# Performance work log

Hardware: AMD Instinct MI355X
Metric: run time of the kernel (lower is better)

## Reference

```python
import jax, jax.numpy as jnp
import numpy as np

N, E = 50000, 800000
DIN, FIN, H, DN, FE = 128, 7, 4, 64, 32
NEG_SLOPE = 0.01  # torch leaky_relu default


def setup_inputs() -> dict:
    key = jax.random.key(0)
    ks = jax.random.split(key, 8)
    nfeats = jax.random.normal(ks[0], (N, DIN), dtype=jnp.float32)
    efeats = jax.random.uniform(ks[1], (E, FIN), dtype=jnp.float32)
    src = jax.random.randint(ks[2], (E,), 0, N, dtype=jnp.int32)
    dst = jax.random.randint(ks[3], (E,), 0, N, dtype=jnp.int32)
    # parameters (xavier-normal-ish scale), stored in jax [in, out] layout
    W_nodes = jax.random.normal(ks[4], (DIN, H * DN), dtype=jnp.float32) * (2.0 / (DIN + H * DN)) ** 0.5
    b_nodes = jnp.zeros((H * DN,), dtype=jnp.float32)
    W_edges = jax.random.normal(ks[5], (FIN + 2 * DIN, H * FE), dtype=jnp.float32) * (2.0 / (FIN + 2 * DIN + H * FE)) ** 0.5
    W_attn = jax.random.normal(ks[6], (H, FE), dtype=jnp.float32) * (2.0 / (FE + H)) ** 0.5  # torch [out,in] layout
    return {"nfeats": nfeats, "efeats": efeats, "src": src, "dst": dst,
            "W_nodes": W_nodes, "b_nodes": b_nodes, "W_edges": W_edges, "W_attn": W_attn}


def reference(nfeats, efeats, src, dst, W_nodes, b_nodes, W_edges, W_attn):
    n = nfeats.shape[0]
    e = efeats.shape[0]
    h_heads = W_attn.shape[0]
    # node projection: [N, H, DN]
    h = (nfeats @ W_nodes + b_nodes).reshape(n, h_heads, -1)
    # per-edge feature MLP on [h_src || f || h_dst]  (raw node feats, as in edge_attention)
    stack = jnp.concatenate([nfeats[src], efeats, nfeats[dst]], axis=-1)  # [E, FIN+2*DIN]
    f_out = jax.nn.leaky_relu(stack @ W_edges, NEG_SLOPE).reshape(e, h_heads, -1)  # [E, H, FE]
    # a = fc_attn(f_out).sum(-1): sums over both attn output heads and FE
    a = jnp.einsum('ehj,kj->eh', f_out, W_attn)  # [E, H]
    # segment (per-destination) softmax, numerically stable
    amax = jax.ops.segment_max(a, dst, num_segments=n)          # [N, H]
    ex = jnp.exp(a - amax[dst])                                 # [E, H]
    denom = jax.ops.segment_sum(ex, dst, num_segments=n)       # [N, H]
    alpha = ex / denom[dst]                                     # [E, H]
    # weighted aggregation of projected src features
    msg = alpha[:, :, None] * h[src]                            # [E, H, DN]
    h_out = jax.ops.segment_sum(msg, dst, num_segments=n)      # [N, H, DN]
    return h_out, f_out
```

## Files before the change

kernel.cpp:

```cpp
#include <hip/hip_runtime.h>

#define NEG_SLOPE 0.01f

typedef __attribute__((ext_vector_type(8))) __bf16 bf16x8;
typedef __attribute__((ext_vector_type(4))) float  f32x4;

__device__ __forceinline__ unsigned short f2bf(float x) {
    unsigned u; __builtin_memcpy(&u, &x, 4);
    unsigned r = u + 0x7FFFu + ((u >> 16) & 1u);
    return (unsigned short)(r >> 16);
}
__device__ __forceinline__ float bflo(unsigned u) {
    unsigned v = u << 16; float f; __builtin_memcpy(&f, &v, 4); return f;
}
__device__ __forceinline__ float bfhi(unsigned u) {
    unsigned v = u & 0xFFFF0000u; float f; __builtin_memcpy(&f, &v, 4); return f;
}

__global__ void zero_kernel(int* __restrict__ p, int n) {
    int i = blockIdx.x * blockDim.x + threadIdx.x;
    if (i < n) p[i] = 0;
}

__global__ __launch_bounds__(256) void bt_prep(
    const float* __restrict__ Wn, const float* __restrict__ We,
    short* __restrict__ Btg)
{
    int idx = blockIdx.x * 256 + threadIdx.x;
    int n = idx >> 7, k = idx & 127;
    float v;
    if (n < 256)      v = Wn[(size_t)k * 256 + n];
    else if (n < 384) v = We[(size_t)k * 128 + (n - 256)];
    else              v = We[(size_t)(135 + k) * 128 + (n - 384)];
    Btg[(size_t)n * 128 + k] = (short)f2bf(v);
}

__global__ __launch_bounds__(256) void gemm_mfma(
    const float* __restrict__ A, const float* __restrict__ bn,
    const short* __restrict__ Btg, unsigned short* __restrict__ hbf,
    unsigned short* __restrict__ Pbf, unsigned short* __restrict__ Qbf, int N)
{
    __shared__ __align__(16) short Al[128 * 136];
    __shared__ __align__(16) short Bl[128 * 136];
    int t = threadIdx.x;
    int row0 = blockIdx.x * 128;

    #pragma unroll
    for (int i = 0; i < 16; i++) {
        int idx = t + i * 256;
        int fr = idx >> 5, fc4 = idx & 31;
        int row = row0 + fr;
        float4 v = make_float4(0.f, 0.f, 0.f, 0.f);
        if (row < N) v = *(const float4*)(A + (size_t)row * 128 + fc4 * 4);
        unsigned long long pk =  (unsigned long long)f2bf(v.x)
                              | ((unsigned long long)f2bf(v.y) << 16)
                              | ((unsigned long long)f2bf(v.z) << 32)
                              | ((unsigned long long)f2bf(v.w) << 48);
        *(unsigned long long*)&Al[fr * 136 + fc4 * 4] = pk;
    }
    __syncthreads();

    int w = t >> 6, l = t & 63;
    int lr = l & 15, lg = l >> 4;

    for (int ct = 0; ct < 4; ct++) {
        if (ct > 0) __syncthreads();
        #pragma unroll
        for (int i = 0; i < 8; i++) {
            int idx = t + i * 256;
            int r = idx >> 4, c8 = idx & 15;
            uint4 v = *(const uint4*)(Btg + (size_t)(ct * 128 + r) * 128 + c8 * 8);
            *(uint4*)&Bl[r * 136 + c8 * 8] = v;
        }
        __syncthreads();

        f32x4 acc[2][8];
        #pragma unroll
        for (int fr = 0; fr < 2; fr++)
            #pragma unroll
            for (int fc = 0; fc < 8; fc++) {
                acc[fr][fc][0] = 0.f; acc[fr][fc][1] = 0.f;
                acc[fr][fc][2] = 0.f; acc[fr][fc][3] = 0.f;
            }

        #pragma unroll
        for (int ks = 0; ks < 4; ks++) {
            int k0 = ks * 32 + lg * 8;
            bf16x8 a0 = *(const bf16x8*)&Al[(w * 32 + lr) * 136 + k0];
            bf16x8 a1 = *(const bf16x8*)&Al[(w * 32 + 16 + lr) * 136 + k0];
            #pragma unroll
            for (int fc = 0; fc < 8; fc++) {
                bf16x8 bb = *(const bf16x8*)&Bl[(fc * 16 + lr) * 136 + k0];
                acc[0][fc] = __builtin_amdgcn_mfma_f32_16x16x32_bf16(a0, bb, acc[0][fc], 0, 0, 0);
                acc[1][fc] = __builtin_amdgcn_mfma_f32_16x16x32_bf16(a1, bb, acc[1][fc], 0, 0, 0);
            }
        }

        #pragma unroll
        for (int fc = 0; fc < 8; fc++) {
            int col = fc * 16 + lr;
            float bias = (ct < 2) ? bn[ct * 128 + col] : 0.f;
            #pragma unroll
            for (int fr = 0; fr < 2; fr++) {
                #pragma unroll
                for (int b = 0; b < 4; b++) {
                    int row = row0 + w * 32 + fr * 16 + lg * 4 + b;
                    if (row >= N) continue;
                    unsigned short bv = f2bf(acc[fr][fc][b] + bias);
                    if (ct < 2)       hbf[(size_t)row * 256 + ct * 128 + col] = bv;
                    else if (ct == 2) Pbf[(size_t)row * 128 + col] = bv;
                    else              Qbf[(size_t)row * 128 + col] = bv;
                }
            }
        }
    }
}

__global__ void count_kernel(const int* __restrict__ dst, int* __restrict__ deg, int E) {
    int i = blockIdx.x * blockDim.x + threadIdx.x;
    if (i < E) atomicAdd(&deg[dst[i]], 1);
}

__global__ __launch_bounds__(256) void scan_sum(
    const int* __restrict__ deg, int* __restrict__ bsum, int n)
{
    int b = blockIdx.x, t = threadIdx.x;
    int base = b * 1024 + t * 4;
    int s = 0;
    #pragma unroll
    for (int k = 0; k < 4; k++) { int i = base + k; if (i < n) s += deg[i]; }
    #pragma unroll
    for (int off = 32; off >= 1; off >>= 1) s += __shfl_xor(s, off);
    __shared__ int ws[4];
    if ((t & 63) == 0) ws[t >> 6] = s;
    __syncthreads();
    if (t == 0) bsum[b] = ws[0] + ws[1] + ws[2] + ws[3];
}

__global__ void scan_offsets(const int* __restrict__ bsum, int* __restrict__ boff,
                             int nb, int* __restrict__ row_start, int n)
{
    int acc = 0;
    for (int b = 0; b < nb; b++) { boff[b] = acc; acc += bsum[b]; }
    row_start[n] = acc;
}

__global__ __launch_bounds__(256) void scan_write(
    const int* __restrict__ deg, const int* __restrict__ boff,
    int* __restrict__ row_start, int* __restrict__ cursor, int n)
{
    int b = blockIdx.x, t = threadIdx.x, lane = t & 63, w = t >> 6;
    int base = b * 1024 + t * 4;
    int x0, x1, x2, x3;
    x0 = (base + 0 < n) ? deg[base + 0] : 0;
    x1 = (base + 1 < n) ? deg[base + 1] : 0;
    x2 = (base + 2 < n) ? deg[base + 2] : 0;
    x3 = (base + 3 < n) ? deg[base + 3] : 0;
    int tsum = x0 + x1 + x2 + x3;
    int inc = tsum;
    #pragma unroll
    for (int off = 1; off < 64; off <<= 1) {
        int v = __shfl_up(inc, off);
        if (lane >= off) inc += v;
    }
    int texcl = inc - tsum;
    __shared__ int wsum[4];
    if (lane == 63) wsum[w] = inc;
    __syncthreads();
    int wexcl = 0;
    #pragma unroll
    for (int ww = 0; ww < 4; ww++) if (ww < w) wexcl += wsum[ww];
    int basev = boff[b] + wexcl + texcl;
    int p0 = basev;
    int p1 = p0 + x0;
    int p2 = p1 + x1;
    int p3 = p2 + x2;
    if (base + 0 < n) { row_start[base + 0] = p0; cursor[base + 0] = p0; }
    if (base + 1 < n) { row_start[base + 1] = p1; cursor[base + 1] = p1; }
    if (base + 2 < n) { row_start[base + 2] = p2; cursor[base + 2] = p2; }
    if (base + 3 < n) { row_start[base + 3] = p3; cursor[base + 3] = p3; }
}

__global__ void scatter_kernel(const int* __restrict__ dst, const int* __restrict__ src,
                               int* __restrict__ cursor, int2* __restrict__ es, int E) {
    int i = blockIdx.x * blockDim.x + threadIdx.x;
    if (i < E) {
        int pos = atomicAdd(&cursor[dst[i]], 1);
        es[pos] = make_int2(i, src[i]);
    }
}

__global__ __launch_bounds__(256) void fused_kernel(
    const int* __restrict__ row_start, const int2* __restrict__ ES,
    const float* __restrict__ ef,
    const unsigned short* __restrict__ Pbf, const unsigned short* __restrict__ Qbf,
    const unsigned short* __restrict__ hbf,
    const float* __restrict__ We, const float* __restrict__ Wa,
    float* __restrict__ f_out, float* __restrict__ out, int N)
{
    int t = threadIdx.x;
    int lane = t & 63;
    int n = (int)((blockIdx.x * blockDim.x + t) >> 6);
    if (n >= N) return;
    int c0 = lane * 2;

    float4* O4 = (float4*)out;
    int nu = __builtin_amdgcn_readfirstlane(n);
    int start = row_start[nu];
    int deg   = row_start[nu + 1] - start;
    if (deg == 0) {
        O4[(size_t)n * 64 + lane] = make_float4(0.f, 0.f, 0.f, 0.f);
        return;
    }

    float wf0[7], wf1[7];
    #pragma unroll
    for (int j = 0; j < 7; j++) {
        wf0[j] = We[(size_t)(128 + j) * 128 + c0];
        wf1[j] = We[(size_t)(128 + j) * 128 + c0 + 1];
    }
    int j0 = c0 & 31, j1 = j0 + 1;
    float wv0 = Wa[j0] + Wa[32 + j0] + Wa[64 + j0] + Wa[96 + j0];
    float wv1 = Wa[j1] + Wa[32 + j1] + Wa[64 + j1] + Wa[96 + j1];

    const unsigned* P1 = (const unsigned*)Pbf;
    const uint2*    H2 = (const uint2*)hbf;

    unsigned qu = ((const unsigned*)Qbf)[(size_t)n * 64 + lane];
    float q0 = bflo(qu), q1 = bfhi(qu);

    #define DSTR(X) \
        float m##X = -1e30f, d##X = 0.f;                                  \
        float4 a##X = make_float4(0.f, 0.f, 0.f, 0.f);                    \
        int e##X = 0; unsigned pu##X = 0; uint2 hu##X = make_uint2(0u,0u);\
        float f##X##0=0.f,f##X##1=0.f,f##X##2=0.f,f##X##3=0.f,            \
              f##X##4=0.f,f##X##5=0.f,f##X##6=0.f;
    #define DNXT(X) \
        int e##X = 0; unsigned pu##X = 0; uint2 hu##X = make_uint2(0u,0u);\
        float f##X##0=0.f,f##X##1=0.f,f##X##2=0.f,f##X##3=0.f,            \
              f##X##4=0.f,f##X##5=0.f,f##X##6=0.f;

    #define LOADE(pos, X) {                                               \
        int p_ = start + (pos);                                           \
        int2 es_ = ES[p_];                                                \
        e##X = __builtin_amdgcn_readfirstlane(es_.x);                     \
        int s_ = __builtin_amdgcn_readfirstlane(es_.y);                   \
        pu##X = P1[(size_t)s_ * 64 + lane];                               \
        hu##X = H2[(size_t)s_ * 64 + lane];                               \
        const float* ep_ = ef + (size_t)e##X * 7;                         \
        f##X##0 = ep_[0]; f##X##1 = ep_[1]; f##X##2 = ep_[2];             \
        f##X##3 = ep_[3]; f##X##4 = ep_[4]; f##X##5 = ep_[5];             \
        f##X##6 = ep_[6]; }

    #define PROC(X) {                                                     \
        float a0 = bflo(pu##X) + q0, a1 = bfhi(pu##X) + q1;               \
        a0 = fmaf(f##X##0, wf0[0], a0); a1 = fmaf(f##X##0, wf1[0], a1);   \
        a0 = fmaf(f##X##1, wf0[1], a0); a1 = fmaf(f##X##1, wf1[1], a1);   \
        a0 = fmaf(f##X##2, wf0[2], a0); a1 = fmaf(f##X##2, wf1[2], a1);   \
        a0 = fmaf(f##X##3, wf0[3], a0); a1 = fmaf(f##X##3, wf1[3], a1);   \
        a0 = fmaf(f##X##4, wf0[4], a0); a1 = fmaf(f##X##4, wf1[4], a1);   \
        a0 = fmaf(f##X##5, wf0[5], a0); a1 = fmaf(f##X##5, wf1[5], a1);   \
        a0 = fmaf(f##X##6, wf0[6], a0); a1 = fmaf(f##X##6, wf1[6], a1);   \
        float v0 = a0 > 0.f ? a0 : NEG_SLOPE * a0;                        \
        float v1 = a1 > 0.f ? a1 : NEG_SLOPE * a1;                        \
        float2 fv_ = make_float2(v0, v1);                                 \
        unsigned long long u_;                                            \
        __builtin_memcpy(&u_, &fv_, 8);                                   \
        __builtin_nontemporal_store(u_,                                   \
            (unsigned long long*)(f_out + (size_t)e##X * 128 + c0));      \
        float p_ = fmaf(v0, wv0, v1 * wv1);                               \
        p_ += __shfl_xor(p_, 8);                                          \
        p_ += __shfl_xor(p_, 4);                                          \
        p_ += __shfl_xor(p_, 2);                                          \
        p_ += __shfl_xor(p_, 1);                                          \
        float nm_ = fmaxf(m##X, p_);                                      \
        float sc_ = __expf(m##X - nm_);                                   \
        float pe_ = __expf(p_ - nm_);                                     \
        d##X = d##X * sc_ + pe_;                                          \
        float hx0 = bflo(hu##X.x), hx1 = bfhi(hu##X.x);                   \
        float hx2 = bflo(hu##X.y), hx3 = bfhi(hu##X.y);                   \
        a##X.x = fmaf(a##X.x, sc_, pe_ * hx0);                            \
        a##X.y = fmaf(a##X.y, sc_, pe_ * hx1);                            \
        a##X.z = fmaf(a##X.z, sc_, pe_ * hx2);                            \
        a##X.w = fmaf(a##X.w, sc_, pe_ * hx3);                            \
        m##X = nm_; }

    #define ROT(X, Y) { e##X = e##Y; pu##X = pu##Y; hu##X = hu##Y;        \
        f##X##0 = f##Y##0; f##X##1 = f##Y##1; f##X##2 = f##Y##2;          \
        f##X##3 = f##Y##3; f##X##4 = f##Y##4; f##X##5 = f##Y##5;          \
        f##X##6 = f##Y##6; }

    DSTR(A) DSTR(B) DSTR(C) DSTR(D)

    LOADE(0, A);
    if (deg > 1) LOADE(1, B);
    if (deg > 2) LOADE(2, C);
    if (deg > 3) LOADE(3, D);

    for (int k = 0;; k++) {
        int base = 4 * k;
        DNXT(An) DNXT(Bn) DNXT(Cn) DNXT(Dn)
        if (base + 4 < deg) LOADE(base + 4, An);
        if (base + 5 < deg) LOADE(base + 5, Bn);
        if (base + 6 < deg) LOADE(base + 6, Cn);
        if (base + 7 < deg) LOADE(base + 7, Dn);

        PROC(A);
        if (base + 1 < deg) PROC(B);
        if (base + 2 < deg) PROC(C);
        if (base + 3 < deg) PROC(D);

        if (base + 4 >= deg) break;
        ROT(A, An); ROT(B, Bn); ROT(C, Cn); ROT(D, Dn);
    }

    float nm = fmaxf(fmaxf(mA, mB), fmaxf(mC, mD));
    float scA = __expf(mA - nm), scB = __expf(mB - nm);
    float scC = __expf(mC - nm), scD = __expf(mD - nm);
    float den = dA * scA + dB * scB + dC * scC + dD * scD;
    float r = 1.f / den;
    float4 acc;
    acc.x = (aA.x * scA + aB.x * scB + aC.x * scC + aD.x * scD) * r;
    acc.y = (aA.y * scA + aB.y * scB + aC.y * scC + aD.y * scD) * r;
    acc.z = (aA.z * scA + aB.z * scB + aC.z * scC + aD.z * scD) * r;
    acc.w = (aA.w * scA + aB.w * scB + aC.w * scC + aD.w * scD) * r;
    O4[(size_t)n * 64 + lane] = acc;

    #undef DSTR
    #undef DNXT
    #undef LOADE
    #undef PROC
    #undef ROT
}

extern "C" void kernel_launch(void* const* d_in, const int* in_sizes, int n_in,
                              void* d_out, int out_size, void* d_ws, size_t ws_size,
                              hipStream_t stream)
{
    const float* nfeats = (const float*)d_in[0];
    const float* efeats = (const float*)d_in[1];
    const int*   src    = (const int*)d_in[2];
    const int*   dst    = (const int*)d_in[3];
    const float* Wn     = (const float*)d_in[4];
    const float* bn     = (const float*)d_in[5];
    const float* We     = (const float*)d_in[6];
    const float* Wa     = (const float*)d_in[7];

    int N = in_sizes[0] / 128;
    int E = in_sizes[2];

    char* ws = (char*)d_ws;
    size_t off = 0;
    unsigned short* hbf = (unsigned short*)(ws + off); off += (size_t)N * 256 * 2;
    unsigned short* Pbf = (unsigned short*)(ws + off); off += (size_t)N * 128 * 2;
    unsigned short* Qbf = (unsigned short*)(ws + off); off += (size_t)N * 128 * 2;
    short* Btg   = (short*)(ws + off); off += (size_t)512 * 128 * 2;
    int2* es       = (int2*)(ws + off); off += (size_t)E * 8;
    int* deg       = (int*)(ws + off); off += (size_t)(N + 1) * 4;
    int* row_start = (int*)(ws + off); off += (size_t)(N + 1) * 4;
    int* cursor    = (int*)(ws + off); off += (size_t)(N + 1) * 4;
    int* bsum      = (int*)(ws + off); off += 1024;
    int* boff      = (int*)(ws + off); off += 1024;

    float* h_out = (float*)d_out;
    float* f_out = (float*)d_out + (size_t)N * 256;

    zero_kernel<<<(N + 255) / 256, 256, 0, stream>>>(deg, N);

    bt_prep<<<256, 256, 0, stream>>>(Wn, We, Btg);
    gemm_mfma<<<(N + 127) / 128, 256, 0, stream>>>(nfeats, bn, Btg, hbf, Pbf, Qbf, N);

    count_kernel<<<(E + 255) / 256, 256, 0, stream>>>(dst, deg, E);

    int nb = (N + 1023) / 1024;
    scan_sum<<<nb, 256, 0, stream>>>(deg, bsum, N);
    scan_offsets<<<1, 1, 0, stream>>>(bsum, boff, nb, row_start, N);
    scan_write<<<nb, 256, 0, stream>>>(deg, boff, row_start, cursor, N);

    scatter_kernel<<<(E + 255) / 256, 256, 0, stream>>>(dst, src, cursor, es, E);

    fused_kernel<<<(N + 3) / 4, 256, 0, stream>>>(row_start, es, efeats,
                                                  Pbf, Qbf, hbf, We, Wa,
                                                  f_out, h_out, N);
}
```

Measured before the change: 327.3 us.

## Interleave P and h rows into one buffer and split GEMM over column tiles

The per-source projections P (128 bf16) and h (256 bf16) now sit in one interleaved row of 384 bf16. Each lane fetches its P pair and h quad with a single 12-byte load, so the gather in the edge loop touches one contiguous region per source node. The GEMM grid also becomes 2D with 64-row tiles and one column tile per block, which gives more blocks and more parallelism, but each column tile reloads and reconverts the A rows. The interleaved write pattern scatters 2-byte stores and the 12-byte gather loads may not be aligned.

```diff
diff --git a/kernel.cpp b/kernel.cpp
--- a/kernel.cpp
+++ b/kernel.cpp
@@ -37,16 +37,17 @@
 
 __global__ __launch_bounds__(256) void gemm_mfma(
     const float* __restrict__ A, const float* __restrict__ bn,
-    const short* __restrict__ Btg, unsigned short* __restrict__ hbf,
-    unsigned short* __restrict__ Pbf, unsigned short* __restrict__ Qbf, int N)
-{
-    __shared__ __align__(16) short Al[128 * 136];
+    const short* __restrict__ Btg, unsigned short* __restrict__ PH,
+    unsigned short* __restrict__ Qbf, int N)
+{
+    __shared__ __align__(16) short Al[64 * 136];
     __shared__ __align__(16) short Bl[128 * 136];
     int t = threadIdx.x;
-    int row0 = blockIdx.x * 128;
-
-    #pragma unroll
-    for (int i = 0; i < 16; i++) {
+    int ct = blockIdx.y;
+    int row0 = blockIdx.x * 64;
+
+    #pragma unroll
+    for (int i = 0; i < 8; i++) {
         int idx = t + i * 256;
         int fr = idx >> 5, fc4 = idx & 31;
         int row = row0 + fr;
@@ -58,59 +59,51 @@
                               | ((unsigned long long)f2bf(v.w) << 48);
         *(unsigned long long*)&Al[fr * 136 + fc4 * 4] = pk;
     }
+    #pragma unroll
+    for (int i = 0; i < 8; i++) {
+        int idx = t + i * 256;
+        int r = idx >> 4, c8 = idx & 15;
+        uint4 v = *(const uint4*)(Btg + (size_t)(ct * 128 + r) * 128 + c8 * 8);
+        *(uint4*)&Bl[r * 136 + c8 * 8] = v;
+    }
     __syncthreads();
 
     int w = t >> 6, l = t & 63;
     int lr = l & 15, lg = l >> 4;
 
-    for (int ct = 0; ct < 4; ct++) {
-        if (ct > 0) __syncthreads();
-        #pragma unroll
-        for (int i = 0; i < 8; i++) {
-            int idx = t + i * 256;
-            int r = idx >> 4, c8 = idx & 15;
-            uint4 v = *(const uint4*)(Btg + (size_t)(ct * 128 + r) * 128 + c8 * 8);
-            *(uint4*)&Bl[r * 136 + c8 * 8] = v;
-        }
-        __syncthreads();
-
-        f32x4 acc[2][8];
-        #pragma unroll
-        for (int fr = 0; fr < 2; fr++)
-            #pragma unroll
-            for (int fc = 0; fc < 8; fc++) {
-                acc[fr][fc][0] = 0.f; acc[fr][fc][1] = 0.f;
-                acc[fr][fc][2] = 0.f; acc[fr][fc][3] = 0.f;
-            }
-
-        #pragma unroll
-        for (int ks = 0; ks < 4; ks++) {
-            int k0 = ks * 32 + lg * 8;
-            bf16x8 a0 = *(const bf16x8*)&Al[(w * 32 + lr) * 136 + k0];
-            bf16x8 a1 = *(const bf16x8*)&Al[(w * 32 + 16 + lr) * 136 + k0];
-            #pragma unroll
-            for (int fc = 0; fc < 8; fc++) {
-                bf16x8 bb = *(const bf16x8*)&Bl[(fc * 16 + lr) * 136 + k0];
-                acc[0][fc] = __builtin_amdgcn_mfma_f32_16x16x32_bf16(a0, bb, acc[0][fc], 0, 0, 0);
-                acc[1][fc] = __builtin_amdgcn_mfma_f32_16x16x32_bf16(a1, bb, acc[1][fc], 0, 0, 0);
-            }
-        }
-
+    f32x4 acc[8];
+    #pragma unroll
+    for (int fc = 0; fc < 8; fc++) {
+        acc[fc][0] = 0.f; acc[fc][1] = 0.f; acc[fc][2] = 0.f; acc[fc][3] = 0.f;
+    }
+
+    #pragma unroll
+    for (int ks = 0; ks < 4; ks++) {
+        int k0 = ks * 32 + lg * 8;
+        bf16x8 a0 = *(const bf16x8*)&Al[(w * 16 + lr) * 136 + k0];
         #pragma unroll
         for (int fc = 0; fc < 8; fc++) {
-            int col = fc * 16 + lr;
-            float bias = (ct < 2) ? bn[ct * 128 + col] : 0.f;
-            #pragma unroll
-            for (int fr = 0; fr < 2; fr++) {
-                #pragma unroll
-                for (int b = 0; b < 4; b++) {
-                    int row = row0 + w * 32 + fr * 16 + lg * 4 + b;
-                    if (row >= N) continue;
-                    unsigned short bv = f2bf(acc[fr][fc][b] + bias);
-                    if (ct < 2)       hbf[(size_t)row * 256 + ct * 128 + col] = bv;
-                    else if (ct == 2) Pbf[(size_t)row * 128 + col] = bv;
-                    else              Qbf[(size_t)row * 128 + col] = bv;
-                }
+            bf16x8 bb = *(const bf16x8*)&Bl[(fc * 16 + lr) * 136 + k0];
+            acc[fc] = __builtin_amdgcn_mfma_f32_16x16x32_bf16(a0, bb, acc[fc], 0, 0, 0);
+        }
+    }
+
+    #pragma unroll
+    for (int fc = 0; fc < 8; fc++) {
+        int col = fc * 16 + lr;
+        float bias = (ct < 2) ? bn[ct * 128 + col] : 0.f;
+        #pragma unroll
+        for (int b = 0; b < 4; b++) {
+            int row = row0 + w * 16 + lg * 4 + b;
+            if (row >= N) continue;
+            unsigned short bv = f2bf(acc[fc][b] + bias);
+            if (ct < 2) {
+                int col256 = ct * 128 + col;
+                PH[(size_t)row * 384 + (col256 >> 2) * 6 + 2 + (col256 & 3)] = bv;
+            } else if (ct == 2) {
+                PH[(size_t)row * 384 + (col >> 1) * 6 + (col & 1)] = bv;
+            } else {
+                Qbf[(size_t)row * 128 + col] = bv;
             }
         }
     }
@@ -193,8 +186,7 @@
 __global__ __launch_bounds__(256) void fused_kernel(
     const int* __restrict__ row_start, const int2* __restrict__ ES,
     const float* __restrict__ ef,
-    const unsigned short* __restrict__ Pbf, const unsigned short* __restrict__ Qbf,
-    const unsigned short* __restrict__ hbf,
+    const unsigned short* __restrict__ PH, const unsigned short* __restrict__ Qbf,
     const float* __restrict__ We, const float* __restrict__ Wa,
     float* __restrict__ f_out, float* __restrict__ out, int N)
 {
@@ -222,9 +214,6 @@
     int j0 = c0 & 31, j1 = j0 + 1;
     float wv0 = Wa[j0] + Wa[32 + j0] + Wa[64 + j0] + Wa[96 + j0];
     float wv1 = Wa[j1] + Wa[32 + j1] + Wa[64 + j1] + Wa[96 + j1];
-
-    const unsigned* P1 = (const unsigned*)Pbf;
-    const uint2*    H2 = (const uint2*)hbf;
 
     unsigned qu = ((const unsigned*)Qbf)[(size_t)n * 64 + lane];
     float q0 = bflo(qu), q1 = bfhi(qu);
@@ -245,8 +234,9 @@
         int2 es_ = ES[p_];                                                \
         e##X = __builtin_amdgcn_readfirstlane(es_.x);                     \
         int s_ = __builtin_amdgcn_readfirstlane(es_.y);                   \
-        pu##X = P1[(size_t)s_ * 64 + lane];                               \
-        hu##X = H2[(size_t)s_ * 64 + lane];                               \
+        uint3 ph_ = *(const uint3*)(PH + (size_t)s_ * 384 + lane * 6);    \
+        pu##X = ph_.x;                                                    \
+        hu##X = make_uint2(ph_.y, ph_.z);                                 \
         const float* ep_ = ef + (size_t)e##X * 7;                         \
         f##X##0 = ep_[0]; f##X##1 = ep_[1]; f##X##2 = ep_[2];             \
         f##X##3 = ep_[3]; f##X##4 = ep_[4]; f##X##5 = ep_[5];             \
@@ -351,8 +341,7 @@
 
     char* ws = (char*)d_ws;
     size_t off = 0;
-    unsigned short* hbf = (unsigned short*)(ws + off); off += (size_t)N * 256 * 2;
-    unsigned short* Pbf = (unsigned short*)(ws + off); off += (size_t)N * 128 * 2;
+    unsigned short* PH  = (unsigned short*)(ws + off); off += (size_t)N * 384 * 2;
     unsigned short* Qbf = (unsigned short*)(ws + off); off += (size_t)N * 128 * 2;
     short* Btg   = (short*)(ws + off); off += (size_t)512 * 128 * 2;
     int2* es       = (int2*)(ws + off); off += (size_t)E * 8;
@@ -368,7 +357,9 @@
     zero_kernel<<<(N + 255) / 256, 256, 0, stream>>>(deg, N);
 
     bt_prep<<<256, 256, 0, stream>>>(Wn, We, Btg);
-    gemm_mfma<<<(N + 127) / 128, 256, 0, stream>>>(nfeats, bn, Btg, hbf, Pbf, Qbf, N);
+
+    dim3 g2((N + 63) / 64, 4);
+    gemm_mfma<<<g2, 256, 0, stream>>>(nfeats, bn, Btg, PH, Qbf, N);
 
     count_kernel<<<(E + 255) / 256, 256, 0, stream>>>(dst, deg, E);
 
@@ -380,6 +371,6 @@
     scatter_kernel<<<(E + 255) / 256, 256, 0, stream>>>(dst, src, cursor, es, E);
 
     fused_kernel<<<(N + 3) / 4, 256, 0, stream>>>(row_start, es, efeats,
-                                                  Pbf, Qbf, hbf, We, Wa,
+                                                  PH, Qbf, We, Wa,
                                                   f_out, h_out, N);
 }
```

New measurement: 331.2 us. No clear change (+1.2%).
